# Performance work log

Hardware: AMD Instinct MI355X
Metric: run time of the kernel (lower is better)

The kernel has to match this reference:

```python
import jax, jax.numpy as jnp
import numpy as np

N_LAYERS = 4
B, L, D = 2, 2048, 512
H, E = 8, 64          # n_heads = d_model // d_head
DFF = 1024
EPS = 1e-6
MAX_LOG_SCALE = float(np.log(100.0))   # QKNorm max_scale clamp
LOG10 = float(np.log(10.0))            # QKNorm scale init


def rms_norm(x, scale, eps=EPS):
    # matches torch rms_norm: x * (scale * rsqrt(mean(x^2, -1) + eps))
    ms = jnp.mean(jnp.square(x), axis=-1, keepdims=True)
    return x * (scale * jax.lax.rsqrt(ms + eps))


def rope(x):
    # standard rotary embedding over head dim, half-split convention. x: [n,h,l,e]
    e, l = x.shape[-1], x.shape[-2]
    inv = 1.0 / (10000.0 ** (jnp.arange(0, e, 2, dtype=jnp.float32) / e))
    freqs = jnp.arange(l, dtype=jnp.float32)[:, None] * inv[None, :]   # [l, e/2]
    cos, sin = jnp.cos(freqs), jnp.sin(freqs)
    x1, x2 = x[..., : e // 2], x[..., e // 2:]
    return jnp.concatenate([x1 * cos - x2 * sin, x1 * sin + x2 * cos], axis=-1)


def setup_inputs() -> dict:
    key = jax.random.key(0)
    ks = jax.random.split(key, 10)
    s = 0.02
    return {
        "x": jax.random.normal(ks[0], (B, L, D), jnp.float32),
        "cond": jax.random.normal(ks[1], (B, D), jnp.float32),
        "attn_mask": jnp.ones((B, L), jnp.int32),
        # per-layer stacked params (torch Linear(in,out,bias=False) stored as [in,out], y = x @ W)
        "wn_attn": s * jax.random.normal(ks[2], (N_LAYERS, D, D), jnp.float32),      # AdaRMSNorm cond proj (attn)
        "wqkv": s * jax.random.normal(ks[3], (N_LAYERS, D, 3 * D), jnp.float32),
        "qk_scale": jnp.full((N_LAYERS, H), LOG10, jnp.float32),                     # QKNorm per-head log-scale
        "wout": s * jax.random.normal(ks[4], (N_LAYERS, D, D), jnp.float32),
        "wn_ff": s * jax.random.normal(ks[5], (N_LAYERS, D, D), jnp.float32),        # AdaRMSNorm cond proj (ff)
        "wup": s * jax.random.normal(ks[6], (N_LAYERS, D, 2 * DFF), jnp.float32),
        "wdown": s * jax.random.normal(ks[7], (N_LAYERS, DFF, D), jnp.float32),
        "out_scale": jnp.ones((D,), jnp.float32),                                    # final RMSNorm scale
    }


def forward(x, cond, attn_mask, wn_attn, wqkv, qk_scale, wout, wn_ff, wup, wdown, out_scale):
    n, l, d = x.shape
    # mask bias: (attn_mask != 1) * -1e9, repeated 'n l -> n h l s' (query-dim mask, as in source)
    bias = (attn_mask != 1).astype(x.dtype) * -1e9
    bias = bias[:, None, :, None]  # [n,1,l,1] broadcast over heads and key dim

    def block(h_x, p):
        wn_a, w_qkv, qs, w_o, wn_f, w_up, w_dn = p
        # --- self attention ---
        skip = h_x
        y = rms_norm(h_x, (cond @ wn_a + 1.0)[:, None, :])            # AdaRMSNorm
        qkv = y @ w_qkv                                               # [n,l,3d]
        q, k, v = jnp.split(qkv, 3, axis=-1)
        to_heads = lambda t: t.reshape(n, l, H, E).transpose(0, 2, 1, 3)
        q, k, v = to_heads(q), to_heads(k), to_heads(v)
        qs_c = jnp.minimum(qs, MAX_LOG_SCALE)
        hs = jnp.exp(0.5 * qs_c - 0.25 * np.log(E))[:, None, None]    # [H,1,1] QKNorm scale
        q = rope(rms_norm(q, hs))
        k = rope(rms_norm(k, hs))
        scores = jnp.einsum('nhle,nhse->nhls', q, k) / np.sqrt(E) + bias
        attn = jax.nn.softmax(scores, axis=-1)
        o = jnp.einsum('nhls,nhse->nhle', attn, v)
        o = o.transpose(0, 2, 1, 3).reshape(n, l, d)
        h_x = skip + o @ w_o
        # --- GEGLU feed-forward ---
        skip = h_x
        y = rms_norm(h_x, (cond @ wn_f + 1.0)[:, None, :])
        u = y @ w_up
        a, b = jnp.split(u, 2, axis=-1)
        y = a * jax.nn.gelu(b, approximate=False)                     # F.gelu exact
        h_x = skip + y @ w_dn
        return h_x, None

    x, _ = jax.lax.scan(block, x, (wn_attn, wqkv, qk_scale, wout, wn_ff, wup, wdown))
    return rms_norm(x, out_scale)


def reference(x, cond, attn_mask, wn_attn, wqkv, qk_scale, wout, wn_ff, wup, wdown, out_scale):
    return forward(x, cond, attn_mask, wn_attn, wqkv, qk_scale, wout, wn_ff, wup, wdown, out_scale)
```

## Files before the change

kernel.cpp:

```cpp
#include <hip/hip_runtime.h>
#include <hip/hip_bf16.h>

#define NB 2
#define LL 2048
#define DD 512
#define HH 8
#define EE 64
#define DFF 1024
#define NL 4
#define EPS_F 1e-6f

typedef __bf16 bf16x8 __attribute__((ext_vector_type(8)));
typedef __bf16 bf16x4 __attribute__((ext_vector_type(4)));
typedef float f32x4 __attribute__((ext_vector_type(4)));

__device__ __forceinline__ unsigned short f2bf(float f) {
    unsigned int u = __float_as_uint(f);
    unsigned int r = (u + 0x7FFFu + ((u >> 16) & 1u)) >> 16;
    return (unsigned short)r;
}
__device__ __forceinline__ unsigned short f2bf_t(float f) {
    return (unsigned short)(__float_as_uint(f) >> 16);
}
__device__ __forceinline__ void gload16(const void* g, void* l) {
    __builtin_amdgcn_global_load_lds(
        (const __attribute__((address_space(1))) unsigned int*)g,
        (__attribute__((address_space(3))) unsigned int*)l, 16, 0, 0);
}

__global__ void rope_table_kernel(float* __restrict__ cosT, float* __restrict__ sinT) {
    int idx = blockIdx.x * 256 + threadIdx.x;
    if (idx >= LL * 32) return;
    int l = idx >> 5, i = idx & 31;
    float inv = powf(10000.f, -(float)i * (1.f / 32.f));
    float ang = (float)l * inv;
    cosT[idx] = cosf(ang);
    sinT[idx] = sinf(ang);
}

__global__ __launch_bounds__(256) void wcast_all_kernel(const float* __restrict__ wqkv,
                                                        const float* __restrict__ wout,
                                                        const float* __restrict__ wup,
                                                        const float* __restrict__ wdown,
                                                        unsigned short* __restrict__ wt) {
    int bid = blockIdx.x;
    int layer = bid / 2560, rem = bid % 2560;
    const float* W; unsigned short* WT; int K, N, t;
    if (rem < 768)       { W = wqkv  + (size_t)layer * 786432;  WT = wt + (size_t)layer * 786432;            K = 512;  N = 1536; t = rem; }
    else if (rem < 1024) { W = wout  + (size_t)layer * 262144;  WT = wt + 3145728 + (size_t)layer * 262144;  K = 512;  N = 512;  t = rem - 768; }
    else if (rem < 2048) { W = wup   + (size_t)layer * 1048576; WT = wt + 4194304 + (size_t)layer * 1048576; K = 512;  N = 2048; t = rem - 1024; }
    else                 { W = wdown + (size_t)layer * 524288;  WT = wt + 8388608 + (size_t)layer * 524288;  K = 1024; N = 512;  t = rem - 2048; }
    int tn = N / 32;
    int n0 = (t % tn) * 32, k0 = (t / tn) * 32;
    __shared__ float tile[32][33];
    int r = threadIdx.x >> 5, c = threadIdx.x & 31;
#pragma unroll
    for (int i = 0; i < 4; ++i)
        tile[r + 8 * i][c] = W[(size_t)(k0 + r + 8 * i) * N + n0 + c];
    __syncthreads();
#pragma unroll
    for (int i = 0; i < 4; ++i)
        WT[(size_t)(n0 + r + 8 * i) * K + k0 + c] = f2bf(tile[c][r + 8 * i]);
}

__global__ __launch_bounds__(256) void cond_all_kernel(const float* __restrict__ cond,
                                                       const float* __restrict__ wn_attn,
                                                       const float* __restrict__ wn_ff,
                                                       float* __restrict__ s_all) {
    int bid = blockIdx.x;
    int d0 = (bid & 7) * 64;
    int b = (bid >> 3) & 1;
    int which = (bid >> 4) & 1;
    int layer = bid >> 5;
    const float* W = (which ? wn_ff : wn_attn) + (size_t)layer * DD * DD;
    int t = threadIdx.x;
    int d = d0 + (t & 63), kq = t >> 6;
    const float* c = cond + b * DD + kq * 128;
    const float* Wp = W + (size_t)(kq * 128) * DD + d;
    float s = 0.f;
#pragma unroll 8
    for (int j = 0; j < 128; ++j) s = fmaf(c[j], Wp[(size_t)j * DD], s);
    __shared__ float red[4][64];
    red[kq][t & 63] = s;
    __syncthreads();
    if (t < 64) {
        float tot = 1.f + red[0][t] + red[1][t] + red[2][t] + red[3][t];
        s_all[((size_t)(layer * 2 + which) * NB + b) * DD + d0 + t] = tot;
    }
}

__global__ __launch_bounds__(256) void rmsnorm_bf16_kernel(const float* __restrict__ x,
                                                           const float* __restrict__ scale,
                                                           unsigned short* __restrict__ y) {
    int row = blockIdx.x;
    int b = row >> 11;
    int t = threadIdx.x;
    float2 v = ((const float2*)(x + (size_t)row * DD))[t];
    float ss = v.x * v.x + v.y * v.y;
#pragma unroll
    for (int o = 32; o > 0; o >>= 1) ss += __shfl_xor(ss, o);
    __shared__ float red[4];
    if ((t & 63) == 0) red[t >> 6] = ss;
    __syncthreads();
    float tot = red[0] + red[1] + red[2] + red[3];
    float inv = rsqrtf(tot * (1.f / DD) + EPS_F);
    float2 s2 = ((const float2*)(scale + b * DD))[t];
    unsigned int lo = f2bf(v.x * s2.x * inv);
    unsigned int hi = f2bf(v.y * s2.y * inv);
    ((unsigned int*)(y + (size_t)row * DD))[t] = lo | (hi << 16);
}

__global__ __launch_bounds__(256) void rmsnorm_f32_kernel(const float* __restrict__ x,
                                                          const float* __restrict__ scale,
                                                          float* __restrict__ y) {
    int row = blockIdx.x;
    int t = threadIdx.x;
    float2 v = ((const float2*)(x + (size_t)row * DD))[t];
    float ss = v.x * v.x + v.y * v.y;
#pragma unroll
    for (int o = 32; o > 0; o >>= 1) ss += __shfl_xor(ss, o);
    __shared__ float red[4];
    if ((t & 63) == 0) red[t >> 6] = ss;
    __syncthreads();
    float tot = red[0] + red[1] + red[2] + red[3];
    float inv = rsqrtf(tot * (1.f / DD) + EPS_F);
    float2 s2 = ((const float2*)scale)[t];
    float2 o2;
    o2.x = v.x * s2.x * inv;
    o2.y = v.y * s2.y * inv;
    ((float2*)(y + (size_t)row * DD))[t] = o2;
}

template <int BN>
__global__ __launch_bounds__(256) void gemm_bf16_kernel(const unsigned short* __restrict__ A,
                                                        const unsigned short* __restrict__ BT,
                                                        const float* __restrict__ R,
                                                        float* __restrict__ C,
                                                        int M, int N, int K) {
    constexpr int NJ = BN / 32;
    __shared__ __align__(16) unsigned short As[2][128 * 32];
    __shared__ __align__(16) unsigned short Bs[2][BN * 32];
    int tid = threadIdx.x;
    int n0 = blockIdx.x * BN, m0 = blockIdx.y * 128;
    int w = tid >> 6, l = tid & 63;
    int wr = w >> 1, wc = w & 1;
    int kf = 8 * (l >> 4);
    int rf = l & 15;

    auto stage = [&](int buf, int k0) {
#pragma unroll
        for (int u = 0; u < 2; ++u) {
            int c = u * 256 + tid;
            int row = c >> 2, ch = c & 3;
            gload16(A + (size_t)(m0 + row) * K + k0 + ch * 8, &As[buf][c * 8]);
        }
#pragma unroll
        for (int u = 0; u < BN / 64; ++u) {
            int c = u * 256 + tid;
            int row = c >> 2, ch = c & 3;
            gload16(BT + (size_t)(n0 + row) * K + k0 + ch * 8, &Bs[buf][c * 8]);
        }
    };

    f32x4 acc[4][NJ] = {};
    const int nt = K / 32;
    stage(0, 0);
    __syncthreads();

    for (int t = 0; t < nt; ++t) {
        if (t + 1 < nt) stage((t + 1) & 1, (t + 1) * 32);
        int cur = t & 1;
        bf16x8 a[4], b[NJ];
#pragma unroll
        for (int i = 0; i < 4; ++i)
            a[i] = *(const bf16x8*)(&As[cur][(wr * 64 + i * 16 + rf) * 32 + kf]);
#pragma unroll
        for (int j = 0; j < NJ; ++j)
            b[j] = *(const bf16x8*)(&Bs[cur][(wc * (BN / 2) + j * 16 + rf) * 32 + kf]);
#pragma unroll
        for (int i = 0; i < 4; ++i)
#pragma unroll
            for (int j = 0; j < NJ; ++j)
                acc[i][j] = __builtin_amdgcn_mfma_f32_16x16x32_bf16(a[i], b[j], acc[i][j], 0, 0, 0);
        __syncthreads();
    }

    int rl = l >> 4, cl = l & 15;
#pragma unroll
    for (int i = 0; i < 4; ++i)
#pragma unroll
        for (int j = 0; j < NJ; ++j)
#pragma unroll
            for (int r = 0; r < 4; ++r) {
                int row = m0 + wr * 64 + i * 16 + rl * 4 + r;
                int col = n0 + wc * (BN / 2) + j * 16 + cl;
                size_t off = (size_t)row * N + col;
                float v = acc[i][j][r];
                if (R) v += R[off];
                C[off] = v;
            }
}

__global__ __launch_bounds__(256) void gemm_qkv_fused_kernel(const unsigned short* __restrict__ A,
                                                             const unsigned short* __restrict__ BT,
                                                             const float* __restrict__ qs,
                                                             const float* __restrict__ cosT,
                                                             const float* __restrict__ sinT,
                                                             unsigned short* __restrict__ qh,
                                                             unsigned short* __restrict__ kh,
                                                             unsigned short* __restrict__ vt) {
    __shared__ __align__(16) unsigned char smem[128 * 65 * sizeof(float)];
    unsigned short* As = (unsigned short*)smem;
    unsigned short* Bs = (unsigned short*)(smem + 16384);
    float* ex = (float*)smem;
    int tid = threadIdx.x;
    int ct = blockIdx.x, m0 = blockIdx.y * 128;
    int n0 = ct * 64;
    int w = tid >> 6, l = tid & 63;
    int wr = w >> 1, wc = w & 1;
    int kf = 8 * (l >> 4);
    int rf = l & 15;

    auto stage = [&](int buf, int k0) {
#pragma unroll
        for (int u = 0; u < 2; ++u) {
            int c = u * 256 + tid;
            int row = c >> 2, ch = c & 3;
            gload16(A + (size_t)(m0 + row) * DD + k0 + ch * 8, &As[buf * 4096 + c * 8]);
        }
        int c = tid;
        int row = c >> 2, ch = c & 3;
        gload16(BT + (size_t)(n0 + row) * DD + k0 + ch * 8, &Bs[buf * 2048 + c * 8]);
    };

    f32x4 acc[4][2] = {};
    stage(0, 0);
    __syncthreads();
    for (int t = 0; t < 16; ++t) {
        if (t + 1 < 16) stage((t + 1) & 1, (t + 1) * 32);
        int cur = t & 1;
        bf16x8 a[4], b[2];
#pragma unroll
        for (int i = 0; i < 4; ++i)
            a[i] = *(const bf16x8*)(&As[cur * 4096 + (wr * 64 + i * 16 + rf) * 32 + kf]);
#pragma unroll
        for (int j = 0; j < 2; ++j)
            b[j] = *(const bf16x8*)(&Bs[cur * 2048 + (wc * 32 + j * 16 + rf) * 32 + kf]);
#pragma unroll
        for (int i = 0; i < 4; ++i)
#pragma unroll
            for (int j = 0; j < 2; ++j)
                acc[i][j] = __builtin_amdgcn_mfma_f32_16x16x32_bf16(a[i], b[j], acc[i][j], 0, 0, 0);
        __syncthreads();
    }

    int rl = l >> 4, cl = l & 15;
#pragma unroll
    for (int i = 0; i < 4; ++i)
#pragma unroll
        for (int j = 0; j < 2; ++j)
#pragma unroll
            for (int r = 0; r < 4; ++r)
                ex[(wr * 64 + i * 16 + rl * 4 + r) * 65 + wc * 32 + j * 16 + cl] = acc[i][j][r];
    __syncthreads();

    int b = m0 >> 11;
    int lbase = m0 & (LL - 1);
    if (ct < 16) {
        int h = ct & 7;
        bool isq = ct < 8;
        float hsc = expf(0.5f * fminf(qs[h], 4.60517019f) - 1.03972077f) * 0.35355339059f;
        if (isq) hsc *= 1.44269504f;
        unsigned short* dst = (isq ? qh : kh) + ((size_t)(b * HH + h) * LL) * EE;
#pragma unroll 4
        for (int it = 0; it < 32; ++it) {
            int row = w * 32 + it;
            int lloc = lbase + row;
            float v = ex[row * 65 + l];
            float ss = v * v;
#pragma unroll
            for (int d = 1; d < 64; d <<= 1) ss += __shfl_xor(ss, d);
            float inv = hsc * rsqrtf(ss * (1.f / EE) + EPS_F);
            float pr = ex[row * 65 + (l ^ 32)];
            int i2 = l & 31;
            float c = cosT[lloc * 32 + i2], s = sinT[lloc * 32 + i2];
            float vn = v * inv, pn = pr * inv;
            float o = (l < 32) ? (vn * c - pn * s) : (pn * s + vn * c);
            dst[(size_t)lloc * EE + l] = f2bf(o);
        }
    } else {
        int h = ct - 16;
        int bh = b * HH + h;
#pragma unroll 4
        for (int it = 0; it < 16; ++it) {
            int e = w * 16 + it;
            float v0 = ex[(2 * l) * 65 + e];
            float v1 = ex[(2 * l + 1) * 65 + e];
            unsigned int pk = (unsigned int)f2bf(v0) | ((unsigned int)f2bf(v1) << 16);
            *(unsigned int*)(vt + ((size_t)(bh * EE + e)) * LL + lbase + 2 * l) = pk;
        }
    }
}

__global__ __launch_bounds__(256) void gemm_geglu_kernel(const unsigned short* __restrict__ A,
                                                         const unsigned short* __restrict__ BT,
                                                         unsigned short* __restrict__ G) {
    __shared__ __align__(16) unsigned char smem[128 * 65 * sizeof(float)];
    unsigned short* As = (unsigned short*)smem;
    unsigned short* Bs = (unsigned short*)(smem + 16384);
    float* ep = (float*)smem;
    int tid = threadIdx.x;
    int n0 = blockIdx.x * 64, m0 = blockIdx.y * 128;
    int w = tid >> 6, l = tid & 63;
    int wr = w >> 1, wc = w & 1;
    int kf = 8 * (l >> 4);
    int rf = l & 15;

    auto stage = [&](int buf, int k0) {
#pragma unroll
        for (int u = 0; u < 2; ++u) {
            int c = u * 256 + tid;
            int row = c >> 2, ch = c & 3;
            gload16(A + (size_t)(m0 + row) * DD + k0 + ch * 8, &As[buf * 4096 + c * 8]);
            int grow = (row < 64) ? (n0 + row) : (DFF + n0 + row - 64);
            gload16(BT + (size_t)grow * DD + k0 + ch * 8, &Bs[buf * 4096 + c * 8]);
        }
    };

    f32x4 acc[4][4] = {};
    stage(0, 0);
    __syncthreads();

    for (int t = 0; t < 16; ++t) {
        if (t + 1 < 16) stage((t + 1) & 1, (t + 1) * 32);
        int cur = t & 1;
        bf16x8 a[4], b[4];
#pragma unroll
        for (int i = 0; i < 4; ++i)
            a[i] = *(const bf16x8*)(&As[cur * 4096 + (wr * 64 + i * 16 + rf) * 32 + kf]);
#pragma unroll
        for (int j = 0; j < 4; ++j)
            b[j] = *(const bf16x8*)(&Bs[cur * 4096 + (wc * 64 + j * 16 + rf) * 32 + kf]);
#pragma unroll
        for (int i = 0; i < 4; ++i)
#pragma unroll
            for (int j = 0; j < 4; ++j)
                acc[i][j] = __builtin_amdgcn_mfma_f32_16x16x32_bf16(a[i], b[j], acc[i][j], 0, 0, 0);
        __syncthreads();
    }

    int rl = l >> 4, cl = l & 15;
    if (wc == 0) {
#pragma unroll
        for (int i = 0; i < 4; ++i)
#pragma unroll
            for (int j = 0; j < 4; ++j)
#pragma unroll
                for (int r = 0; r < 4; ++r)
                    ep[(wr * 64 + i * 16 + rl * 4 + r) * 65 + j * 16 + cl] = acc[i][j][r];
    }
    __syncthreads();
    if (wc == 1) {
#pragma unroll
        for (int i = 0; i < 4; ++i)
#pragma unroll
            for (int j = 0; j < 4; ++j)
#pragma unroll
                for (int r = 0; r < 4; ++r) {
                    int row = wr * 64 + i * 16 + rl * 4 + r;
                    float bv = acc[i][j][r];
                    float av = ep[row * 65 + j * 16 + cl];
                    float ge = 0.5f * bv * (1.f + erff(bv * 0.70710678f));
                    G[(size_t)(m0 + row) * DFF + n0 + j * 16 + cl] = f2bf(av * ge);
                }
    }
}

#define KVB 32
#define KLDP 72
#define VLDP 40
#define PLDP 36
__global__ __launch_bounds__(256) void flash_mfma_kernel(const unsigned short* __restrict__ qh,
                                                         const unsigned short* __restrict__ kh,
                                                         const unsigned short* __restrict__ vt,
                                                         unsigned short* __restrict__ op,
                                                         float* __restrict__ os) {
    __shared__ unsigned short K_lds[32 * KLDP];
    __shared__ unsigned short VT_lds[80 * VLDP];
    __shared__ unsigned short P_lds[4][16 * PLDP];
    int bid = blockIdx.x;
    int qb = bid & 31, h = (bid >> 5) & 7, b = (bid >> 8) & 1, split = bid >> 9;
    int bh = b * HH + h;
    int tid = threadIdx.x, w = tid >> 6, l = tid & 63;
    int lo = l & 15, hi4 = l >> 4;
    int q0 = qb * 64 + w * 16;

    for (int idx = tid; idx < 16 * VLDP; idx += 256) {
        int rr = idx / VLDP;
        VT_lds[(64 + rr) * VLDP + (idx - rr * VLDP)] = (rr == 0) ? 0x3F80 : 0;
    }

    const unsigned short* qbase = qh + ((size_t)bh * LL) * EE;
    bf16x8 qa[2];
#pragma unroll
    for (int s = 0; s < 2; ++s)
        qa[s] = *(const bf16x8*)(qbase + (size_t)(q0 + lo) * EE + s * 32 + 8 * hi4);

    f32x4 oacc[4] = {};
    f32x4 osum = {};

    for (int kt = split * 16; kt < split * 16 + 16; ++kt) {
        int kv0 = kt * KVB;
#pragma unroll
        for (int u = 0; u < 2; ++u) {
            int c = tid + u * 256;
            int arr = c >> 8, cc = c & 255;
            if (arr == 0) {
                int row = cc >> 3, ch = cc & 7;
                *(uint4*)&K_lds[row * KLDP + ch * 8] =
                    *(const uint4*)(kh + ((size_t)bh * LL + kv0 + row) * EE + ch * 8);
            } else {
                int row = cc >> 2, ch = cc & 3;
                *(uint4*)&VT_lds[row * VLDP + ch * 8] =
                    *(const uint4*)(vt + ((size_t)bh * EE + row) * LL + kv0 + ch * 8);
            }
        }
        __syncthreads();

        f32x4 S[2] = {};
        __builtin_amdgcn_s_setprio(1);
#pragma unroll
        for (int nf = 0; nf < 2; ++nf)
#pragma unroll
            for (int s = 0; s < 2; ++s) {
                bf16x8 kb = *(const bf16x8*)&K_lds[(nf * 16 + lo) * KLDP + s * 32 + 8 * hi4];
                S[nf] = __builtin_amdgcn_mfma_f32_16x16x32_bf16(qa[s], kb, S[nf], 0, 0, 0);
            }
        __builtin_amdgcn_s_setprio(0);

#pragma unroll
        for (int r = 0; r < 4; ++r)
#pragma unroll
            for (int nf = 0; nf < 2; ++nf)
                P_lds[w][(hi4 * 4 + r) * PLDP + nf * 16 + lo] = f2bf_t(exp2f(S[nf][r]));

        __builtin_amdgcn_s_setprio(1);
        bf16x4 p0 = *(const bf16x4*)&P_lds[w][lo * PLDP + 8 * hi4];
        bf16x4 p1 = *(const bf16x4*)&P_lds[w][lo * PLDP + 8 * hi4 + 4];
        bf16x8 pa;
#pragma unroll
        for (int j = 0; j < 4; ++j) { pa[j] = p0[j]; pa[4 + j] = p1[j]; }
#pragma unroll
        for (int nf = 0; nf < 4; ++nf) {
            bf16x8 vb = *(const bf16x8*)&VT_lds[(nf * 16 + lo) * VLDP + 8 * hi4];
            oacc[nf] = __builtin_amdgcn_mfma_f32_16x16x32_bf16(pa, vb, oacc[nf], 0, 0, 0);
        }
        bf16x8 vbE = *(const bf16x8*)&VT_lds[(64 + lo) * VLDP + 8 * hi4];
        osum = __builtin_amdgcn_mfma_f32_16x16x32_bf16(pa, vbE, osum, 0, 0, 0);
        __builtin_amdgcn_s_setprio(0);
        __syncthreads();
    }

    unsigned short* opp = op + (size_t)split * (NB * LL * DD);
#pragma unroll
    for (int r = 0; r < 4; ++r) {
        int row = q0 + hi4 * 4 + r;
        unsigned short* optr = opp + ((size_t)(b * LL + row)) * DD + h * EE;
#pragma unroll
        for (int nf = 0; nf < 4; ++nf)
            optr[nf * 16 + lo] = f2bf(oacc[nf][r]);
        if (lo == 0)
            os[split * (NB * HH * LL) + bh * LL + row] = osum[r];
    }
}

__global__ __launch_bounds__(256) void attn_combine_kernel(const unsigned short* __restrict__ op,
                                                           const float* __restrict__ os,
                                                           unsigned short* __restrict__ oh) {
    int idx = (blockIdx.x * 256 + threadIdx.x) * 8;
    int col = idx & 511;
    int h = col >> 6;
    int row = (idx >> 9) & (LL - 1);
    int b = idx >> 20;
    int bh = b * HH + h;
    float s = 0.f;
    float a[8] = {};
#pragma unroll
    for (int sp = 0; sp < 4; ++sp) {
        s += os[sp * (NB * HH * LL) + bh * LL + row];
        uint4 t = *(const uint4*)(op + (size_t)sp * (NB * LL * DD) + idx);
        unsigned int dw[4] = {t.x, t.y, t.z, t.w};
#pragma unroll
        for (int j = 0; j < 4; ++j) {
            a[2 * j]     += __uint_as_float(dw[j] << 16);
            a[2 * j + 1] += __uint_as_float(dw[j] & 0xFFFF0000u);
        }
    }
    float inv = 1.f / s;
    uint4 o4;
    unsigned int* po = (unsigned int*)&o4;
#pragma unroll
    for (int j = 0; j < 4; ++j)
        po[j] = (unsigned int)f2bf(a[2 * j] * inv) | ((unsigned int)f2bf(a[2 * j + 1] * inv) << 16);
    *(uint4*)(oh + idx) = o4;
}

extern "C" void kernel_launch(void* const* d_in, const int* in_sizes, int n_in,
                              void* d_out, int out_size, void* d_ws, size_t ws_size,
                              hipStream_t stream) {
    const float* x        = (const float*)d_in[0];
    const float* cond     = (const float*)d_in[1];
    const float* wn_attn  = (const float*)d_in[3];
    const float* wqkv     = (const float*)d_in[4];
    const float* qk_scale = (const float*)d_in[5];
    const float* wout     = (const float*)d_in[6];
    const float* wn_ff    = (const float*)d_in[7];
    const float* wup      = (const float*)d_in[8];
    const float* wdown    = (const float*)d_in[9];
    const float* out_scale= (const float*)d_in[10];
    float* out = (float*)d_out;

    const int TOK = NB * LL;
    const size_t nHx = (size_t)TOK * DD;
    const size_t M = 1024 * 1024;

    float* ws = (float*)d_ws;
    float* hx  = ws;
    unsigned short* y_bf = (unsigned short*)(ws + 2 * M);
    unsigned short* op   = (unsigned short*)(ws + 3 * M);
    unsigned short* qh_bf = (unsigned short*)(ws + 11 * M);
    unsigned short* g_bf  = (unsigned short*)(ws + 11 * M);
    unsigned short* kh_bf = (unsigned short*)(ws + 12 * M);
    unsigned short* vt_bf = (unsigned short*)(ws + 13 * M);
    unsigned short* oh_bf = (unsigned short*)(ws + 14 * M);
    unsigned short* wt = (unsigned short*)(ws + 15 * M);
    float* smal  = ws + 20 * M;
    float* s_all = smal;
    float* os    = smal + 8192;
    float* cosT  = os + 131072;
    float* sinT  = cosT + 65536;

    hipMemcpyAsync(hx, x, nHx * sizeof(float), hipMemcpyDeviceToDevice, stream);
    rope_table_kernel<<<256, 256, 0, stream>>>(cosT, sinT);
    cond_all_kernel<<<128, 256, 0, stream>>>(cond, wn_attn, wn_ff, s_all);
    wcast_all_kernel<<<10240, 256, 0, stream>>>(wqkv, wout, wup, wdown, wt);

    unsigned short* wqkvT  = wt;
    unsigned short* woutT  = wt + 3145728;
    unsigned short* wupT   = wt + 4194304;
    unsigned short* wdownT = wt + 8388608;

    for (int layer = 0; layer < NL; ++layer) {
        const float* qs = qk_scale + layer * HH;

        rmsnorm_bf16_kernel<<<TOK, 256, 0, stream>>>(hx, s_all + (size_t)(layer * 2 + 0) * NB * DD, y_bf);
        gemm_qkv_fused_kernel<<<dim3(24, TOK / 128), 256, 0, stream>>>(
            y_bf, wqkvT + (size_t)layer * 786432, qs, cosT, sinT, qh_bf, kh_bf, vt_bf);
        flash_mfma_kernel<<<2048, 256, 0, stream>>>(qh_bf, kh_bf, vt_bf, op, os);
        attn_combine_kernel<<<1024, 256, 0, stream>>>(op, os, oh_bf);
        gemm_bf16_kernel<64><<<dim3(512 / 64, TOK / 128), 256, 0, stream>>>(
            oh_bf, woutT + (size_t)layer * 262144, hx, hx, TOK, 512, 512);

        rmsnorm_bf16_kernel<<<TOK, 256, 0, stream>>>(hx, s_all + (size_t)(layer * 2 + 1) * NB * DD, y_bf);
        gemm_geglu_kernel<<<dim3(16, 32), 256, 0, stream>>>(
            y_bf, wupT + (size_t)layer * 1048576, g_bf);
        gemm_bf16_kernel<64><<<dim3(512 / 64, TOK / 128), 256, 0, stream>>>(
            g_bf, wdownT + (size_t)layer * 524288, hx, hx, TOK, 512, 1024);
    }
    rmsnorm_f32_kernel<<<TOK, 256, 0, stream>>>(hx, out_scale, out);
}
```

Measured before the change: 577.7 us.

## Double-buffer K/V tiles in flash attention with register prefetch

The flash attention kernel now keeps two LDS buffers for the K and V^T tiles. Each iteration issues the global loads for the next tile into registers before computing on the current one, then writes them to the other buffer after the MFMAs. This drops one barrier per iteration and hides global load latency behind compute. The cost is more LDS use and more registers, which may lower occupancy.

```diff
diff --git a/kernel.cpp b/kernel.cpp
--- a/kernel.cpp
+++ b/kernel.cpp
@@ -385,8 +385,9 @@
                                                          const unsigned short* __restrict__ vt,
                                                          unsigned short* __restrict__ op,
                                                          float* __restrict__ os) {
-    __shared__ unsigned short K_lds[32 * KLDP];
-    __shared__ unsigned short VT_lds[80 * VLDP];
+    __shared__ unsigned short K_lds[2][32 * KLDP];
+    __shared__ unsigned short VT_lds[2][64 * VLDP];
+    __shared__ unsigned short S_lds[16 * VLDP];
     __shared__ unsigned short P_lds[4][16 * PLDP];
     int bid = blockIdx.x;
     int qb = bid & 31, h = (bid >> 5) & 7, b = (bid >> 8) & 1, split = bid >> 9;
@@ -397,7 +398,7 @@
 
     for (int idx = tid; idx < 16 * VLDP; idx += 256) {
         int rr = idx / VLDP;
-        VT_lds[(64 + rr) * VLDP + (idx - rr * VLDP)] = (rr == 0) ? 0x3F80 : 0;
+        S_lds[idx] = (rr == 0) ? 0x3F80 : 0;
     }
 
     const unsigned short* qbase = qh + ((size_t)bh * LL) * EE;
@@ -406,34 +407,40 @@
     for (int s = 0; s < 2; ++s)
         qa[s] = *(const bf16x8*)(qbase + (size_t)(q0 + lo) * EE + s * 32 + 8 * hi4);
 
+    int krow = tid >> 3, kch = tid & 7;
+    int vrow = tid >> 2, vch = tid & 3;
+    const uint4* gK = (const uint4*)(kh + ((size_t)bh * LL + split * 16 * KVB + krow) * EE + kch * 8);
+    const uint4* gV = (const uint4*)(vt + ((size_t)bh * EE + vrow) * LL + split * 16 * KVB + vch * 8);
+    const int gKstep = KVB * EE / 8;
+    const int gVstep = KVB / 8;
+    unsigned short* ldsK = &K_lds[0][krow * KLDP + kch * 8];
+    unsigned short* ldsV = &VT_lds[0][vrow * VLDP + vch * 8];
+    const int ldsKsz = 32 * KLDP, ldsVsz = 64 * VLDP;
+
+    uint4 pk = *gK, pv = *gV;
+    *(uint4*)ldsK = pk;
+    *(uint4*)ldsV = pv;
+    __syncthreads();
+
     f32x4 oacc[4] = {};
     f32x4 osum = {};
 
-    for (int kt = split * 16; kt < split * 16 + 16; ++kt) {
-        int kv0 = kt * KVB;
-#pragma unroll
-        for (int u = 0; u < 2; ++u) {
-            int c = tid + u * 256;
-            int arr = c >> 8, cc = c & 255;
-            if (arr == 0) {
-                int row = cc >> 3, ch = cc & 7;
-                *(uint4*)&K_lds[row * KLDP + ch * 8] =
-                    *(const uint4*)(kh + ((size_t)bh * LL + kv0 + row) * EE + ch * 8);
-            } else {
-                int row = cc >> 2, ch = cc & 3;
-                *(uint4*)&VT_lds[row * VLDP + ch * 8] =
-                    *(const uint4*)(vt + ((size_t)bh * EE + row) * LL + kv0 + ch * 8);
-            }
-        }
-        __syncthreads();
-
+    for (int t = 0; t < 16; ++t) {
+        int cur = t & 1;
+        if (t + 1 < 16) {
+            pk = gK[(t + 1) * gKstep];
+            pv = gV[(t + 1) * gVstep];
+        }
+
+        const unsigned short* Kc = &K_lds[cur][0];
+        const unsigned short* Vc = &VT_lds[cur][0];
         f32x4 S[2] = {};
         __builtin_amdgcn_s_setprio(1);
 #pragma unroll
         for (int nf = 0; nf < 2; ++nf)
 #pragma unroll
             for (int s = 0; s < 2; ++s) {
-                bf16x8 kb = *(const bf16x8*)&K_lds[(nf * 16 + lo) * KLDP + s * 32 + 8 * hi4];
+                bf16x8 kb = *(const bf16x8*)&Kc[(nf * 16 + lo) * KLDP + s * 32 + 8 * hi4];
                 S[nf] = __builtin_amdgcn_mfma_f32_16x16x32_bf16(qa[s], kb, S[nf], 0, 0, 0);
             }
         __builtin_amdgcn_s_setprio(0);
@@ -452,12 +459,17 @@
         for (int j = 0; j < 4; ++j) { pa[j] = p0[j]; pa[4 + j] = p1[j]; }
 #pragma unroll
         for (int nf = 0; nf < 4; ++nf) {
-            bf16x8 vb = *(const bf16x8*)&VT_lds[(nf * 16 + lo) * VLDP + 8 * hi4];
+            bf16x8 vb = *(const bf16x8*)&Vc[(nf * 16 + lo) * VLDP + 8 * hi4];
             oacc[nf] = __builtin_amdgcn_mfma_f32_16x16x32_bf16(pa, vb, oacc[nf], 0, 0, 0);
         }
-        bf16x8 vbE = *(const bf16x8*)&VT_lds[(64 + lo) * VLDP + 8 * hi4];
+        bf16x8 vbE = *(const bf16x8*)&S_lds[lo * VLDP + 8 * hi4];
         osum = __builtin_amdgcn_mfma_f32_16x16x32_bf16(pa, vbE, osum, 0, 0, 0);
         __builtin_amdgcn_s_setprio(0);
+
+        if (t + 1 < 16) {
+            *(uint4*)(ldsK + (cur ^ 1) * ldsKsz) = pk;
+            *(uint4*)(ldsV + (cur ^ 1) * ldsVsz) = pv;
+        }
         __syncthreads();
     }
 
```

New measurement: 571.9 us. Within noise of the previous version (-1.0%).
